# Kernel tuning notes

Measured on AMD Instinct MI355X. Metric: run time of the kernel, lower is better.

The kernel has to match this reference:

```python
import jax, jax.numpy as jnp
import numpy as np

NEG_SLOPE = 0.2  # PyG GATConv default negative_slope


def gat_conv(x, W, b, a_src, a_dst, src, dst, N, H, C):
    """PyG-style GATConv (v1 attention), concat heads, self-loops already in (src,dst)."""
    h = (x @ W).reshape(N, H, C)                       # [N,H,C]
    al_src = jnp.sum(h * a_src, axis=-1)               # [N,H]
    al_dst = jnp.sum(h * a_dst, axis=-1)               # [N,H]
    e = jax.nn.leaky_relu(al_src[src] + al_dst[dst], NEG_SLOPE)  # [E,H]
    m = jax.ops.segment_max(e, dst, num_segments=N)    # segment softmax (stable)
    m = jnp.where(jnp.isfinite(m), m, 0.0)
    ex = jnp.exp(e - m[dst])
    denom = jax.ops.segment_sum(ex, dst, num_segments=N)
    alpha = ex / (denom[dst] + 1e-16)                  # [E,H]
    msg = h[src] * alpha[..., None]                    # [E,H,C]
    out = jax.ops.segment_sum(msg, dst, num_segments=N)  # [N,H,C]
    return out.reshape(N, H * C) + b


def setup_inputs() -> dict:
    key = jax.random.key(0)
    ks = jax.random.split(key, 16)
    N, E, IN, HID, HEADS, OUT, G = 50000, 600000, 128, 64, 4, 10, 64
    x = jax.random.normal(ks[0], (N, IN), dtype=jnp.float32)
    edge_index = jax.random.randint(ks[1], (2, E), 0, N, dtype=jnp.int32)
    batch = jnp.sort(jax.random.randint(ks[2], (N,), 0, G, dtype=jnp.int32))
    s = 0.1
    p = {
        'W1': jax.random.normal(ks[3], (IN, HEADS * HID)) * s,
        'b1': jnp.zeros((HEADS * HID,), jnp.float32),
        'asrc1': jax.random.normal(ks[4], (HEADS, HID)) * s,
        'adst1': jax.random.normal(ks[5], (HEADS, HID)) * s,
        'W2': jax.random.normal(ks[6], (HEADS * HID, HEADS * HID)) * s,
        'b2': jnp.zeros((HEADS * HID,), jnp.float32),
        'asrc2': jax.random.normal(ks[7], (HEADS, HID)) * s,
        'adst2': jax.random.normal(ks[8], (HEADS, HID)) * s,
        'W3': jax.random.normal(ks[9], (HEADS * HID, HID)) * s,
        'b3': jnp.zeros((HID,), jnp.float32),
        'asrc3': jax.random.normal(ks[10], (1, HID)) * s,
        'adst3': jax.random.normal(ks[11], (1, HID)) * s,
        'linW': jax.random.normal(ks[12], (HID, OUT)) * s,
        'linb': jnp.zeros((OUT,), jnp.float32),
    }
    return dict(x=x, edge_index=edge_index, batch=batch, **p)


def reference(x, edge_index, batch, W1, b1, asrc1, adst1, W2, b2, asrc2, adst2,
              W3, b3, asrc3, adst3, linW, linb):
    N = x.shape[0]
    G = 64  # number of graphs
    loops = jnp.arange(N, dtype=edge_index.dtype)
    src = jnp.concatenate([edge_index[0], loops])  # PyG adds self-loops by default
    dst = jnp.concatenate([edge_index[1], loops])
    # eval mode: dropout is identity
    h = jax.nn.elu(gat_conv(x, W1, b1, asrc1, adst1, src, dst, N, 4, 64))
    h = jax.nn.elu(gat_conv(h, W2, b2, asrc2, adst2, src, dst, N, 4, 64))
    h = jax.nn.elu(gat_conv(h, W3, b3, asrc3, adst3, src, dst, N, 1, 64))
    # global mean pool over graphs
    sums = jax.ops.segment_sum(h, batch, num_segments=G)            # [G,64]
    cnts = jax.ops.segment_sum(jnp.ones((N,), h.dtype), batch, num_segments=G)
    pooled = sums / jnp.maximum(cnts, 1.0)[:, None]
    return pooled @ linW + linb                                      # [G,10]
```

## Files before the change

### kernel.cpp

```cpp
#include <hip/hip_runtime.h>
#include <hip/hip_bf16.h>
#include <math.h>

#define NEG_SLOPE 0.2f

typedef short short8 __attribute__((ext_vector_type(8)));
typedef float f32x4 __attribute__((ext_vector_type(4)));
typedef unsigned int u32;
typedef unsigned short u16;

__device__ __forceinline__ float lrelu(float x){ return x > 0.f ? x : NEG_SLOPE * x; }
__device__ __forceinline__ float elu_f(float x){ return x > 0.f ? x : __expf(x) - 1.f; }
__device__ __forceinline__ u16 f2bf(float f){
  __hip_bfloat16 h = __float2bfloat16(f);
  return *(u16*)&h;
}

__global__ void prep_kernel(const float* __restrict__ x, u16* __restrict__ xb, int n4,
                            const float* __restrict__ W1, u16* __restrict__ w1t,
                            const float* __restrict__ W2, u16* __restrict__ w2t,
                            const float* __restrict__ W3, u16* __restrict__ w3t,
                            int* __restrict__ cursor, int N){
  int i = blockIdx.x * 256 + threadIdx.x;
  if (i < n4){
    float4 v = ((const float4*)x)[i];
    ushort4 o;
    o.x = f2bf(v.x); o.y = f2bf(v.y); o.z = f2bf(v.z); o.w = f2bf(v.w);
    ((ushort4*)xb)[i] = o;
    return;
  }
  int t = i - n4;
  if (t < 128 * 256){
    int k = t >> 8, m = t & 255;
    w1t[m * 128 + k] = f2bf(W1[t]);
    return;
  }
  t -= 128 * 256;
  if (t < 256 * 256){
    int k = t >> 8, m = t & 255;
    w2t[m * 256 + k] = f2bf(W2[t]);
    return;
  }
  t -= 256 * 256;
  if (t < 256 * 64){
    int k = t >> 6, m = t & 63;
    w3t[m * 256 + k] = f2bf(W3[t]);
    return;
  }
  t -= 256 * 64;
  if (t < N) cursor[t] = 0;
}

__global__ void ell_kernel(const int* __restrict__ src, const int* __restrict__ dst,
                           int E, int N, int* cursor, int* __restrict__ ell){
  int i = blockIdx.x * 256 + threadIdx.x;
  if (i < E + N){
    int s, d;
    if (i < E){ s = src[i]; d = dst[i]; }
    else      { s = i - E;  d = i - E;  }
    int pos = atomicAdd(&cursor[d], 1);
    if (pos < 64) ell[(size_t)d * 64 + pos] = s;
  }
}

template<int BN>
__global__ __launch_bounds__(256) void gemm_mfma(const u16* __restrict__ A,
                                                 const u16* __restrict__ Bt,
                                                 u16* __restrict__ C,
                                                 const float* __restrict__ asrc,
                                                 const float* __restrict__ adst,
                                                 float* __restrict__ als,
                                                 float* __restrict__ ald,
                                                 int N, int K, int M){
  constexpr int BM = 128;
  constexpr int MI = (BN == 128) ? 4 : 2;
  constexpr int SB = BN * 8 / 256;
  constexpr int HH = (BN == 128) ? 4 : 1;
  __shared__ short As[8][BM][8];
  __shared__ short Bs[8][BN][8];
  const int tid = threadIdx.x;
  const int w = tid >> 6, lane = tid & 63;
  const int quad = lane >> 4, l16 = lane & 15;
  const int row0 = blockIdx.y * BM, col0 = blockIdx.x * BN;
  const int wrow = (BN == 128) ? (w >> 1) * 64 : w * 32;
  const int wcol = (BN == 128) ? (w & 1) * 64 : 0;

  f32x4 acc[MI][4];
#pragma unroll
  for (int i = 0; i < MI; i++)
#pragma unroll
    for (int j = 0; j < 4; j++) acc[i][j] = (f32x4){0.f, 0.f, 0.f, 0.f};

  for (int k0 = 0; k0 < K; k0 += 64){
    __syncthreads();
#pragma unroll
    for (int q = 0; q < 4; q++){
      int lb = q * 256 + w * 64;
      int li = lb + lane;
      int c = li >> 7, r = li & 127;
      int grow = min(row0 + r, N - 1);
      const u16* gp = A + (size_t)grow * K + k0 + c * 8;
      __builtin_amdgcn_global_load_lds((const __attribute__((address_space(1))) void*)gp,
                                       (__attribute__((address_space(3))) void*)((char*)&As[0][0][0] + (size_t)lb * 16),
                                       16, 0, 0);
    }
#pragma unroll
    for (int q = 0; q < SB; q++){
      int lb = q * 256 + w * 64;
      int li = lb + lane;
      int c = li / BN, n = li % BN;
      const u16* gp = Bt + (size_t)(col0 + n) * K + k0 + c * 8;
      __builtin_amdgcn_global_load_lds((const __attribute__((address_space(1))) void*)gp,
                                       (__attribute__((address_space(3))) void*)((char*)&Bs[0][0][0] + (size_t)lb * 16),
                                       16, 0, 0);
    }
    __syncthreads();
#pragma unroll
    for (int ks = 0; ks < 2; ks++){
      short8 a[MI], b[4];
#pragma unroll
      for (int i = 0; i < MI; i++) a[i] = *(const short8*)&As[ks * 4 + quad][wrow + i * 16 + l16][0];
#pragma unroll
      for (int j = 0; j < 4; j++)  b[j] = *(const short8*)&Bs[ks * 4 + quad][wcol + j * 16 + l16][0];
#pragma unroll
      for (int i = 0; i < MI; i++)
#pragma unroll
        for (int j = 0; j < 4; j++)
          acc[i][j] = __builtin_amdgcn_mfma_f32_16x16x32_bf16(a[i], b[j], acc[i][j], 0, 0, 0);
    }
  }

  const int head = (col0 + wcol) >> 6;
  float avs[4], avd[4];
#pragma unroll
  for (int j = 0; j < 4; j++){
    int c = j * 16 + l16;
    avs[j] = asrc[head * 64 + c];
    avd[j] = adst[head * 64 + c];
  }

#pragma unroll
  for (int i = 0; i < MI; i++){
#pragma unroll
    for (int rr = 0; rr < 4; rr++){
      int row = row0 + wrow + i * 16 + quad * 4 + rr;
      float ps = acc[i][0][rr] * avs[0] + acc[i][1][rr] * avs[1]
               + acc[i][2][rr] * avs[2] + acc[i][3][rr] * avs[3];
      float pd = acc[i][0][rr] * avd[0] + acc[i][1][rr] * avd[1]
               + acc[i][2][rr] * avd[2] + acc[i][3][rr] * avd[3];
#pragma unroll
      for (int off = 8; off > 0; off >>= 1){
        ps += __shfl_xor(ps, off);
        pd += __shfl_xor(pd, off);
      }
      if (row < N){
#pragma unroll
        for (int j = 0; j < 4; j++)
          C[(size_t)row * M + col0 + wcol + j * 16 + l16] = f2bf(acc[i][j][rr]);
        if (l16 == 0){
          als[(size_t)row * HH + head] = ps;
          ald[(size_t)row * HH + head] = pd;
        }
      }
    }
  }
}

template<bool OBF>
__global__ __launch_bounds__(256) void agg4_kernel(const u16* __restrict__ hb,
    const float* __restrict__ als, const float* __restrict__ ald,
    const int* __restrict__ degv, const int* __restrict__ ell,
    const float* __restrict__ bias, void* __restrict__ outv, int N){
  __shared__ float lex[4][256];
  __shared__ int lu[4][64];
  int wslot = threadIdx.x >> 6;
  int node = (blockIdx.x * 256 + threadIdx.x) >> 6;
  int lane = threadIdx.x & 63;
  if (node >= N) return;
  int deg = degv[node];
  float4 t4 = *(const float4*)(ald + node * 4);
  const int hh = lane >> 4;

  bool v = lane < deg;
  int u_raw = ell[(size_t)node * 64 + lane];
  int u = v ? u_raw : 0;
  float4 s = *(const float4*)(als + (size_t)u * 4);
  float4 exv;
  exv.x = v ? __expf(lrelu(s.x + t4.x)) : 0.f;
  exv.y = v ? __expf(lrelu(s.y + t4.y)) : 0.f;
  exv.z = v ? __expf(lrelu(s.z + t4.z)) : 0.f;
  exv.w = v ? __expf(lrelu(s.w + t4.w)) : 0.f;
  *(float4*)&lex[wslot][lane * 4] = exv;
  lu[wslot][lane] = u;
  asm volatile("s_waitcnt lgkmcnt(0)" ::: "memory");

  float a0 = 0.f, a1 = 0.f, a2 = 0.f, a3 = 0.f, denom = 0.f;
  const u16* hbl = hb + lane * 4;
#pragma unroll 8
  for (int jj = 0; jj < deg; jj++){
    float ex = lex[wslot][jj * 4 + hh];
    int uu = lu[wslot][jj];
    uint2 t = *(const uint2*)(hbl + (size_t)uu * 256);
    denom += ex;
    a0 += ex * __uint_as_float((t.x & 0xffffu) << 16);
    a1 += ex * __uint_as_float(t.x & 0xffff0000u);
    a2 += ex * __uint_as_float((t.y & 0xffffu) << 16);
    a3 += ex * __uint_as_float(t.y & 0xffff0000u);
  }
  float inv = 1.f / (denom + 1e-16f);
  int ch = lane * 4;
  float o0 = elu_f(a0 * inv + bias[ch]);
  float o1 = elu_f(a1 * inv + bias[ch + 1]);
  float o2 = elu_f(a2 * inv + bias[ch + 2]);
  float o3 = elu_f(a3 * inv + bias[ch + 3]);
  if (OBF){
    uint2 o;
    o.x = (u32)f2bf(o0) | ((u32)f2bf(o1) << 16);
    o.y = (u32)f2bf(o2) | ((u32)f2bf(o3) << 16);
    ((uint2*)outv)[(size_t)node * 64 + lane] = o;
  } else {
    *(float4*)((float*)outv + (size_t)node * 256 + ch) = make_float4(o0, o1, o2, o3);
  }
}

__global__ __launch_bounds__(256) void agg1_kernel(const u16* __restrict__ hb,
    const float* __restrict__ als, const float* __restrict__ ald,
    const int* __restrict__ degv, const int* __restrict__ ell,
    const float* __restrict__ bias, float* __restrict__ out, int N){
  __shared__ float lex[4][72];
  __shared__ int lu[4][72];
  int wslot = threadIdx.x >> 6;
  int node = (blockIdx.x * 256 + threadIdx.x) >> 6;
  int lane = threadIdx.x & 63;
  if (node >= N) return;
  int deg = degv[node];
  float adv = ald[node];

  bool v = lane < deg;
  int u_raw = ell[(size_t)node * 64 + lane];
  int u = v ? u_raw : 0;
  lex[wslot][lane] = v ? __expf(lrelu(als[u] + adv)) : 0.f;
  lu[wslot][lane] = u;
  if (lane < 8){ lex[wslot][64 + lane] = 0.f; lu[wslot][64 + lane] = 0; }
  asm volatile("s_waitcnt lgkmcnt(0)" ::: "memory");

  int eo = lane >> 4;
  int chb = (lane & 15) * 4;
  float a0 = 0.f, a1 = 0.f, a2 = 0.f, a3 = 0.f, denom = 0.f;
#pragma unroll 4
  for (int j2 = 0; j2 < deg; j2 += 4){
    int jj = j2 + eo;
    float ex = lex[wslot][jj];
    int uu = lu[wslot][jj];
    uint2 t = *(const uint2*)(hb + (size_t)uu * 64 + chb);
    denom += ex;
    a0 += ex * __uint_as_float((t.x & 0xffffu) << 16);
    a1 += ex * __uint_as_float(t.x & 0xffff0000u);
    a2 += ex * __uint_as_float((t.y & 0xffffu) << 16);
    a3 += ex * __uint_as_float(t.y & 0xffff0000u);
  }
#pragma unroll
  for (int off = 16; off < 64; off <<= 1){
    denom += __shfl_xor(denom, off);
    a0 += __shfl_xor(a0, off); a1 += __shfl_xor(a1, off);
    a2 += __shfl_xor(a2, off); a3 += __shfl_xor(a3, off);
  }
  if (eo == 0){
    float inv = 1.f / (denom + 1e-16f);
    float o0 = elu_f(a0 * inv + bias[chb]);
    float o1 = elu_f(a1 * inv + bias[chb + 1]);
    float o2 = elu_f(a2 * inv + bias[chb + 2]);
    float o3 = elu_f(a3 * inv + bias[chb + 3]);
    *(float4*)(out + (size_t)node * 64 + chb) = make_float4(o0, o1, o2, o3);
  }
}

__global__ __launch_bounds__(256) void poolfinal_kernel(const float* __restrict__ f,
    const int* __restrict__ batch, const float* __restrict__ linW,
    const float* __restrict__ linb, float* __restrict__ out, int N){
  __shared__ float red[4][64];
  int g = blockIdx.x;
  int tid = threadIdx.x, w = tid >> 6, lane = tid & 63;
  int lo = 0, hi = N;
  while (lo < hi){ int mid = (lo + hi) >> 1; if (batch[mid] < g) lo = mid + 1; else hi = mid; }
  int start = lo;
  hi = N;
  while (lo < hi){ int mid = (lo + hi) >> 1; if (batch[mid] < g + 1) lo = mid + 1; else hi = mid; }
  int end = lo;

  float acc = 0.f;
  for (int n = start + w; n < end; n += 4) acc += f[(size_t)n * 64 + lane];
  red[w][lane] = acc;
  __syncthreads();
  if (w == 0){
    float pooled = red[0][lane] + red[1][lane] + red[2][lane] + red[3][lane];
    pooled /= fmaxf((float)(end - start), 1.f);
    float p[10];
#pragma unroll
    for (int o = 0; o < 10; o++) p[o] = pooled * linW[lane * 10 + o];
#pragma unroll
    for (int off = 32; off > 0; off >>= 1)
#pragma unroll
      for (int o = 0; o < 10; o++) p[o] += __shfl_xor(p[o], off);
    if (lane < 10) out[g * 10 + lane] = p[lane] + linb[lane];
  }
}

extern "C" void kernel_launch(void* const* d_in, const int* in_sizes, int n_in,
                              void* d_out, int out_size, void* d_ws, size_t ws_size,
                              hipStream_t stream) {
  const float* x     = (const float*)d_in[0];
  const int*   ei    = (const int*)  d_in[1];
  const int*   batch = (const int*)  d_in[2];
  const float* W1    = (const float*)d_in[3];
  const float* b1    = (const float*)d_in[4];
  const float* asrc1 = (const float*)d_in[5];
  const float* adst1 = (const float*)d_in[6];
  const float* W2    = (const float*)d_in[7];
  const float* b2    = (const float*)d_in[8];
  const float* asrc2 = (const float*)d_in[9];
  const float* adst2 = (const float*)d_in[10];
  const float* W3    = (const float*)d_in[11];
  const float* b3    = (const float*)d_in[12];
  const float* asrc3 = (const float*)d_in[13];
  const float* adst3 = (const float*)d_in[14];
  const float* linW  = (const float*)d_in[15];
  const float* linb  = (const float*)d_in[16];

  const int N = in_sizes[0] / 128;
  const int E = in_sizes[1] / 2;
  const int Etot = E + N;
  const int G = 64;
  const int* src = ei;
  const int* dst = ei + E;

  char* p = (char*)d_ws;
  auto carve = [&](size_t bytes) -> char* {
    char* r = p;
    p += (bytes + 255) & ~(size_t)255;
    return r;
  };
  u16*   xb       = (u16*)  carve((size_t)N * 128 * 2);
  u16*   w1t      = (u16*)  carve((size_t)256 * 128 * 2);
  u16*   w2t      = (u16*)  carve((size_t)256 * 256 * 2);
  u16*   w3t      = (u16*)  carve((size_t)64 * 256 * 2);
  u16*   hb       = (u16*)  carve((size_t)N * 256 * 2);
  u16*   featb    = (u16*)  carve((size_t)N * 256 * 2);
  float* out3     = (float*)carve((size_t)N * 64 * 4);
  float* als      = (float*)carve((size_t)N * 4 * 4);
  float* ald      = (float*)carve((size_t)N * 4 * 4);
  int*   cursor   = (int*)  carve((size_t)N * 4);
  int*   ell      = (int*)  carve((size_t)N * 64 * 4);

  const int n4 = N * 128 / 4;
  const int prep_items = n4 + 128 * 256 + 256 * 256 + 256 * 64 + N;

  prep_kernel<<<(prep_items + 255) / 256, 256, 0, stream>>>(x, xb, n4, W1, w1t, W2, w2t, W3, w3t,
                                                            cursor, N);

  ell_kernel<<<(Etot + 255) / 256, 256, 0, stream>>>(src, dst, E, N, cursor, ell);

  const int nby = (N + 127) / 128;
  const int wpn_grid = (N + 3) / 4;

  gemm_mfma<128><<<dim3(2, nby), 256, 0, stream>>>(xb, w1t, hb, asrc1, adst1, als, ald, N, 128, 256);
  agg4_kernel<true><<<wpn_grid, 256, 0, stream>>>(hb, als, ald, cursor, ell, b1, featb, N);

  gemm_mfma<128><<<dim3(2, nby), 256, 0, stream>>>(featb, w2t, hb, asrc2, adst2, als, ald, N, 256, 256);
  agg4_kernel<true><<<wpn_grid, 256, 0, stream>>>(hb, als, ald, cursor, ell, b2, featb, N);

  gemm_mfma<64><<<dim3(1, nby), 256, 0, stream>>>(featb, w3t, hb, asrc3, adst3, als, ald, N, 256, 64);
  agg1_kernel<<<wpn_grid, 256, 0, stream>>>(hb, als, ald, cursor, ell, b3, out3, N);

  poolfinal_kernel<<<G, 256, 0, stream>>>(out3, batch, linW, linb, (float*)d_out, N);
}
```

Before: 383.6 us.

## Split global mean pool into chunked atomic partial sums plus final projection

Replaces the 64-block per-graph pooling kernel with a pool kernel that spreads nodes across about 391 blocks of 128 nodes each. Each block accumulates runs of same-graph nodes and adds them to global sums and counts with atomics, and a separate single-block kernel then applies the mean and the linear layer. The goal is to fix the low parallelism of the old pool, where only 64 blocks each walked about 780 nodes serially. In exchange it adds one kernel launch, zero-initialisation in the prep kernel, and float atomics that make the summation order nondeterministic.

```diff
diff --git a/kernel.cpp b/kernel.cpp
--- a/kernel.cpp
+++ b/kernel.cpp
@@ -20,7 +20,8 @@
                             const float* __restrict__ W1, u16* __restrict__ w1t,
                             const float* __restrict__ W2, u16* __restrict__ w2t,
                             const float* __restrict__ W3, u16* __restrict__ w3t,
-                            int* __restrict__ cursor, int N){
+                            int* __restrict__ cursor, int N,
+                            float* __restrict__ sums, int* __restrict__ cnts){
   int i = blockIdx.x * 256 + threadIdx.x;
   if (i < n4){
     float4 v = ((const float4*)x)[i];
@@ -48,7 +49,11 @@
     return;
   }
   t -= 256 * 64;
-  if (t < N) cursor[t] = 0;
+  if (t < N){ cursor[t] = 0; return; }
+  t -= N;
+  if (t < 64 * 64){ sums[t] = 0.f; return; }
+  t -= 64 * 64;
+  if (t < 64) cnts[t] = 0;
 }
 
 __global__ void ell_kernel(const int* __restrict__ src, const int* __restrict__ dst,
@@ -275,35 +280,40 @@
   }
 }
 
-__global__ __launch_bounds__(256) void poolfinal_kernel(const float* __restrict__ f,
-    const int* __restrict__ batch, const float* __restrict__ linW,
-    const float* __restrict__ linb, float* __restrict__ out, int N){
-  __shared__ float red[4][64];
-  int g = blockIdx.x;
-  int tid = threadIdx.x, w = tid >> 6, lane = tid & 63;
-  int lo = 0, hi = N;
-  while (lo < hi){ int mid = (lo + hi) >> 1; if (batch[mid] < g) lo = mid + 1; else hi = mid; }
-  int start = lo;
-  hi = N;
-  while (lo < hi){ int mid = (lo + hi) >> 1; if (batch[mid] < g + 1) lo = mid + 1; else hi = mid; }
-  int end = lo;
-
+__global__ void pool_kernel(const float* __restrict__ f, const int* __restrict__ batch,
+                            float* sums, int* cnts, int N){
+  int lane = threadIdx.x;
+  int s = blockIdx.x * 128;
+  if (s >= N) return;
+  int e = min(s + 128, N);
   float acc = 0.f;
-  for (int n = start + w; n < end; n += 4) acc += f[(size_t)n * 64 + lane];
-  red[w][lane] = acc;
-  __syncthreads();
-  if (w == 0){
-    float pooled = red[0][lane] + red[1][lane] + red[2][lane] + red[3][lane];
-    pooled /= fmaxf((float)(end - start), 1.f);
-    float p[10];
-#pragma unroll
-    for (int o = 0; o < 10; o++) p[o] = pooled * linW[lane * 10 + o];
-#pragma unroll
-    for (int off = 32; off > 0; off >>= 1)
-#pragma unroll
-      for (int o = 0; o < 10; o++) p[o] += __shfl_xor(p[o], off);
-    if (lane < 10) out[g * 10 + lane] = p[lane] + linb[lane];
-  }
+  int cnt = 0;
+  int cur = batch[s];
+  for (int n = s; n < e; n++){
+    int g = batch[n];
+    if (g != cur){
+      atomicAdd(&sums[cur * 64 + lane], acc);
+      if (lane == 0) atomicAdd(&cnts[cur], cnt);
+      acc = 0.f; cnt = 0; cur = g;
+    }
+    acc += f[(size_t)n * 64 + lane];
+    cnt++;
+  }
+  atomicAdd(&sums[cur * 64 + lane], acc);
+  if (lane == 0) atomicAdd(&cnts[cur], cnt);
+}
+
+__global__ void final_kernel(const float* __restrict__ sums, const int* __restrict__ cnts,
+                             const float* __restrict__ linW, const float* __restrict__ linb,
+                             float* __restrict__ out){
+  int t = threadIdx.x;
+  if (t >= 640) return;
+  int g = t / 10, o = t % 10;
+  float c = fmaxf((float)cnts[g], 1.f);
+  float acc = 0.f;
+#pragma unroll
+  for (int k = 0; k < 64; k++) acc += sums[g * 64 + k] * linW[k * 10 + o];
+  out[t] = acc / c + linb[o];
 }
 
 extern "C" void kernel_launch(void* const* d_in, const int* in_sizes, int n_in,
@@ -351,12 +361,14 @@
   float* ald      = (float*)carve((size_t)N * 4 * 4);
   int*   cursor   = (int*)  carve((size_t)N * 4);
   int*   ell      = (int*)  carve((size_t)N * 64 * 4);
+  float* sums     = (float*)carve((size_t)G * 64 * 4);
+  int*   cnts     = (int*)  carve((size_t)G * 4);
 
   const int n4 = N * 128 / 4;
-  const int prep_items = n4 + 128 * 256 + 256 * 256 + 256 * 64 + N;
+  const int prep_items = n4 + 128 * 256 + 256 * 256 + 256 * 64 + N + G * 64 + G;
 
   prep_kernel<<<(prep_items + 255) / 256, 256, 0, stream>>>(x, xb, n4, W1, w1t, W2, w2t, W3, w3t,
-                                                            cursor, N);
+                                                            cursor, N, sums, cnts);
 
   ell_kernel<<<(Etot + 255) / 256, 256, 0, stream>>>(src, dst, E, N, cursor, ell);
 
@@ -372,5 +384,6 @@
   gemm_mfma<64><<<dim3(1, nby), 256, 0, stream>>>(featb, w3t, hb, asrc3, adst3, als, ald, N, 256, 64);
   agg1_kernel<<<wpn_grid, 256, 0, stream>>>(hb, als, ald, cursor, ell, b3, out3, N);
 
-  poolfinal_kernel<<<G, 256, 0, stream>>>(out3, batch, linW, linb, (float*)d_out, N);
-}
+  pool_kernel<<<(N + 127) / 128, 64, 0, stream>>>(out3, batch, sums, cnts, N);
+  final_kernel<<<1, 640, 0, stream>>>(sums, cnts, linW, linb, (float*)d_out);
+}
```

After: 365.6 us. 1.05x faster.
